# Kernel tuning notes

Hardware: AMD Instinct MI355X
Metric: run time of the kernel (lower is better)

## Reference

```python
import jax, jax.numpy as jnp
import numpy as np

B, S, D = 4, 2048, 1024
H = 16
DH = D // H  # 64
THETA = 10000.0


def setup_inputs() -> dict:
    key = jax.random.key(0)
    ks = jax.random.split(key, 7)
    scale = 1.0 / np.sqrt(D)
    return {
        "Q": jax.random.normal(ks[0], (B, S, D), dtype=jnp.float32),
        "K": jax.random.normal(ks[1], (B, S, D), dtype=jnp.float32),
        "V": jax.random.normal(ks[2], (B, S, D), dtype=jnp.float32),
        "Wq": jax.random.normal(ks[3], (D, D), dtype=jnp.float32) * scale,
        "Wk": jax.random.normal(ks[4], (D, D), dtype=jnp.float32) * scale,
        "Wv": jax.random.normal(ks[5], (D, D), dtype=jnp.float32) * scale,
        "Wo": jax.random.normal(ks[6], (D, D), dtype=jnp.float32) * scale,
    }


def _rope_tables(seq_len, d_head, theta, dtype):
    inv_freq = 1.0 / theta ** (jnp.arange(0, d_head, 2, dtype=jnp.float32) / d_head)
    ang = jnp.arange(seq_len, dtype=jnp.float32)[:, None] * inv_freq[None, :]  # [S, DH/2]
    return jnp.sin(ang).astype(dtype), jnp.cos(ang).astype(dtype)


def _apply_rope(x, sin, cos):
    # x: [B, H, S, DH]; sin/cos: [S, DH/2] broadcast over B,H
    x1 = x[..., 0::2]
    x2 = x[..., 1::2]
    x1r = x1 * cos - x2 * sin
    x2r = x1 * sin + x2 * cos
    return jnp.stack([x1r, x2r], axis=-1).reshape(x.shape)


def reference(Q, K, V, Wq, Wk, Wv, Wo):
    seq_len = Q.shape[-2]
    q = Q @ Wq.T
    k = K @ Wk.T
    v = V @ Wv.T

    def split(x):  # [B, S, D] -> [B, H, S, DH]
        return x.reshape(x.shape[0], seq_len, H, DH).transpose(0, 2, 1, 3)

    qh, kh, vh = split(q), split(k), split(v)

    sin, cos = _rope_tables(seq_len, DH, THETA, qh.dtype)
    qh = _apply_rope(qh, sin, cos)
    kh = _apply_rope(kh, sin, cos)

    # attention in fp32 (matches original cast)
    qf = qh.astype(jnp.float32)
    kf = kh.astype(jnp.float32)
    vf = vh.astype(jnp.float32)
    scale = 1.0 / np.sqrt(DH)
    scores = jnp.einsum('bhqd,bhkd->bhqk', qf, kf) * scale
    causal = jnp.tril(jnp.ones((seq_len, seq_len), dtype=bool))
    scores = jnp.where(causal, scores, -jnp.inf)
    attn = jax.nn.softmax(scores, axis=-1)
    out_h = jnp.einsum('bhqk,bhkd->bhqd', attn, vf).astype(Q.dtype)

    out = out_h.transpose(0, 2, 1, 3).reshape(Q.shape[0], seq_len, D)
    return out @ Wo.T
```

## Files before the change

kernel.cpp:

```cpp
#include <hip/hip_runtime.h>
#include <hip/hip_bf16.h>
#include <cmath>

#define B_ 4
#define S_ 2048
#define D_ 1024
#define H_ 16
#define DH_ 64

typedef __bf16 bf16_t;
typedef __bf16 bf16x8 __attribute__((ext_vector_type(8)));
typedef __bf16 bf16x4 __attribute__((ext_vector_type(4)));
typedef float f32x4 __attribute__((ext_vector_type(4)));

static __device__ __forceinline__ f32x4 mfma16(bf16x8 a, bf16x8 b, f32x4 c) {
    return __builtin_amdgcn_mfma_f32_16x16x32_bf16(a, b, c, 0, 0, 0);
}

static __device__ __forceinline__ float fast_exp2(float x) {
#if __has_builtin(__builtin_amdgcn_exp2f)
    return __builtin_amdgcn_exp2f(x);
#else
    float r; asm("v_exp_f32 %0, %1" : "=v"(r) : "v"(x)); return r;
#endif
}

static __device__ __forceinline__ void glds16(const void* g, void* l) {
    __builtin_amdgcn_global_load_lds(
        (const __attribute__((address_space(1))) unsigned int*)g,
        (__attribute__((address_space(3))) unsigned int*)l, 16, 0, 0);
}

__global__ __launch_bounds__(256)
void prep_kernel(const float* __restrict__ Wq, const float* __restrict__ Wk,
                 const float* __restrict__ Wv, const float* __restrict__ Wo,
                 bf16_t* __restrict__ Wb, float2* __restrict__ tab)
{
    int bid = blockIdx.x;
    if (bid < 256) {
        int idx = bid * 256 + threadIdx.x;
        int s = idx >> 5, i = idx & 31;
        float inv = powf(10000.f, -(2.f * i) / 64.f);
        float ang = (float)s * inv;
        tab[idx] = make_float2(sinf(ang), cosf(ang));
    } else {
        int i = (bid - 256) * 256 + threadIdx.x;
        int t = i >> 17, j = i & 131071;
        const float* src = (t == 0) ? Wq : (t == 1) ? Wk : (t == 2) ? Wv : Wo;
        const float4* s = (const float4*)(src + (size_t)j * 8);
        float4 a = s[0], b = s[1];
        bf16x8 v = { (__bf16)a.x, (__bf16)a.y, (__bf16)a.z, (__bf16)a.w,
                     (__bf16)b.x, (__bf16)b.y, (__bf16)b.z, (__bf16)b.w };
        *(bf16x8*)(Wb + (size_t)i * 8) = v;
    }
}

template<int EPI>
__global__ __launch_bounds__(256)
void proj_kernel(const float* __restrict__ X, const bf16_t* __restrict__ W,
                 bf16_t* __restrict__ dst, const float2* __restrict__ tab)
{
    __shared__ bf16x8 lA[2][128 * 8];
    __shared__ bf16x8 lB[2][128 * 8];
    const int tid = threadIdx.x;
    const int gm0 = blockIdx.x * 128;
    const int gn0 = blockIdx.y * 128;
    const int wid = tid >> 6, lane = tid & 63;
    const int lr = lane & 15, lh = lane >> 4;
    const int wm = (wid >> 1) * 64, wn = (wid & 1) * 64;

    int arow[4], aslot[4];
    const float* abase[4];
    #pragma unroll
    for (int i = 0; i < 4; ++i) {
        int slot = i * 256 + tid;
        int row = slot >> 3, s = slot & 7, c = s ^ (row & 7);
        arow[i] = row; aslot[i] = s;
        abase[i] = X + (size_t)(gm0 + row) * D_ + c * 8;
    }
    const bf16_t* bsrc[4]; int bbase[4];
    #pragma unroll
    for (int i = 0; i < 4; ++i) {
        int base = wid * 64 + i * 256;
        int slot = base + lane;
        int row = slot >> 3, s = slot & 7, c = s ^ (row & 7);
        bbase[i] = base;
        bsrc[i] = W + (size_t)(gn0 + row) * D_ + c * 8;
    }

    float4 av0[4], av1[4];
    #pragma unroll
    for (int i = 0; i < 4; ++i) {
        av0[i] = *(const float4*)(abase[i]);
        av1[i] = *(const float4*)(abase[i] + 4);
    }
    #pragma unroll
    for (int i = 0; i < 4; ++i) glds16(bsrc[i], &lB[0][bbase[i]]);
    #pragma unroll
    for (int i = 0; i < 4; ++i) {
        lA[0][arow[i] * 8 + aslot[i]] = bf16x8{
            (__bf16)av0[i].x, (__bf16)av0[i].y, (__bf16)av0[i].z, (__bf16)av0[i].w,
            (__bf16)av1[i].x, (__bf16)av1[i].y, (__bf16)av1[i].z, (__bf16)av1[i].w };
    }
    __syncthreads();

    f32x4 acc[4][4] = {};
    int cur = 0;

    #pragma unroll 1
    for (int kt = 0; kt < D_ / 64; ++kt) {
        const int nxt = cur ^ 1;
        if (kt + 1 < D_ / 64) {
            #pragma unroll
            for (int i = 0; i < 4; ++i)
                glds16(bsrc[i] + (kt + 1) * 64, &lB[nxt][bbase[i]]);
            #pragma unroll
            for (int i = 0; i < 4; ++i) {
                av0[i] = *(const float4*)(abase[i] + (kt + 1) * 64);
                av1[i] = *(const float4*)(abase[i] + (kt + 1) * 64 + 4);
            }
        }
        #pragma unroll
        for (int ks = 0; ks < 2; ++ks) {
            bf16x8 af[4], bfr[4];
            int kh8 = ks * 4 + lh;
            #pragma unroll
            for (int mi = 0; mi < 4; ++mi) { int r = wm + mi * 16 + lr; af[mi]  = lA[cur][r * 8 + (kh8 ^ (r & 7))]; }
            #pragma unroll
            for (int ni = 0; ni < 4; ++ni) { int r = wn + ni * 16 + lr; bfr[ni] = lB[cur][r * 8 + (kh8 ^ (r & 7))]; }
            #pragma unroll
            for (int mi = 0; mi < 4; ++mi)
                #pragma unroll
                for (int ni = 0; ni < 4; ++ni)
                    acc[mi][ni] = mfma16(af[mi], bfr[ni], acc[mi][ni]);
        }
        if (kt + 1 < D_ / 64) {
            #pragma unroll
            for (int i = 0; i < 4; ++i) {
                lA[nxt][arow[i] * 8 + aslot[i]] = bf16x8{
                    (__bf16)av0[i].x, (__bf16)av0[i].y, (__bf16)av0[i].z, (__bf16)av0[i].w,
                    (__bf16)av1[i].x, (__bf16)av1[i].y, (__bf16)av1[i].z, (__bf16)av1[i].w };
            }
        }
        __syncthreads();
        cur = nxt;
    }

    #pragma unroll
    for (int mi = 0; mi < 4; ++mi) {
        #pragma unroll
        for (int j = 0; j < 4; ++j) {
            int m = gm0 + wm + mi * 16 + lh * 4 + j;
            int b = m >> 11, s = m & (S_ - 1);
            #pragma unroll
            for (int ni = 0; ni < 4; ++ni) {
                int n = gn0 + wn + ni * 16 + lr;
                int h = n >> 6, dh = n & 63;
                float x = acc[mi][ni][j];
                if (EPI == 0) {
                    float p = __shfl_xor(x, 1);
                    float2 sc = tab[s * 32 + (dh >> 1)];
                    float r = (dh & 1) ? (p * sc.x + x * sc.y)
                                       : (x * sc.y - p * sc.x);
                    dst[(((size_t)b * H_ + h) * S_ + s) * DH_ + dh] = (bf16_t)r;
                } else {
                    dst[(((size_t)b * H_ + h) * DH_ + dh) * S_ + s] = (bf16_t)x;
                }
            }
        }
    }
}

__global__ __launch_bounds__(256, 6)
void attn_kernel(const bf16_t* __restrict__ qh, const bf16_t* __restrict__ kh,
                 const bf16_t* __restrict__ vT, bf16_t* __restrict__ O)
{
    __shared__ bf16x8 lK[64 * 8];
    __shared__ bf16x8 lV[64 * 8];
    __shared__ bf16x8 lP8[4][128];
    const int tid = threadIdx.x, wid = tid >> 6, lane = tid & 63;
    const int lr = lane & 15, lh = lane >> 4;
    const int bh = blockIdx.x & 63;
    const int t  = 31 - (blockIdx.x >> 6);
    const bf16_t* Qp = qh + (size_t)bh * S_ * DH_;
    const bf16_t* Kp = kh + (size_t)bh * S_ * DH_;
    const bf16_t* Vp = vT + (size_t)bh * DH_ * S_;
    char* lP = (char*)lP8[wid];
    const int b = bh >> 4, h = bh & 15;
    const float QSCALE = 0.125f * 1.44269504f;
    const int wq = t * 64 + wid * 16;

    bf16x8 qf[2];
    #pragma unroll
    for (int ks = 0; ks < 2; ++ks) {
        bf16x8 q8 = *(const bf16x8*)(Qp + (size_t)(wq + lr) * DH_ + ks * 32 + lh * 8);
        #pragma unroll
        for (int e = 0; e < 8; ++e) q8[e] = (__bf16)((float)q8[e] * QSCALE);
        qf[ks] = q8;
    }

    f32x4 accO[4] = {};
    float mrun = -1e30f, lrun = 0.f;
    const int nkt = t + 1;

    #pragma unroll 1
    for (int kt = 0; kt < nkt; ++kt) {
        __syncthreads();
        #pragma unroll
        for (int i = 0; i < 2; ++i) {
            int base = i * 256 + (wid << 6);
            int slot = base + lane;
            int row = slot >> 3, s = slot & 7, c = s ^ (row & 7);
            glds16(Kp + (size_t)(kt * 64 + row) * DH_ + c * 8, &lK[base]);
            glds16(Vp + (size_t)row * S_ + kt * 64 + c * 8, &lV[base]);
        }
        __syncthreads();

        f32x4 sc[4] = {};
        __builtin_amdgcn_s_setprio(1);
        #pragma unroll
        for (int ks = 0; ks < 2; ++ks) {
            int kh8 = ks * 4 + lh;
            #pragma unroll
            for (int kvi = 0; kvi < 4; ++kvi) {
                int r = kvi * 16 + lr;
                bf16x8 kf = lK[r * 8 + (kh8 ^ (r & 7))];
                sc[kvi] = mfma16(kf, qf[ks], sc[kvi]);
            }
        }
        __builtin_amdgcn_s_setprio(0);

        const int kvb = kt * 64 + 4 * lh;
        const int qg = wq + lr;
        float pv[16];
        if (kt == t) {
            #pragma unroll
            for (int kvi = 0; kvi < 4; ++kvi)
                #pragma unroll
                for (int j = 0; j < 4; ++j) {
                    float x = sc[kvi][j];
                    if ((kvb + kvi * 16 + j) > qg) x = -1e30f;
                    pv[kvi * 4 + j] = x;
                }
        } else {
            #pragma unroll
            for (int kvi = 0; kvi < 4; ++kvi)
                #pragma unroll
                for (int j = 0; j < 4; ++j) pv[kvi * 4 + j] = sc[kvi][j];
        }

        float t0 = fmaxf(fmaxf(pv[0],  pv[1]),  pv[2]);
        float t1 = fmaxf(fmaxf(pv[3],  pv[4]),  pv[5]);
        float t2 = fmaxf(fmaxf(pv[6],  pv[7]),  pv[8]);
        float t3 = fmaxf(fmaxf(pv[9],  pv[10]), pv[11]);
        float t4 = fmaxf(fmaxf(pv[12], pv[13]), pv[14]);
        float u0 = fmaxf(fmaxf(t0, t1), t2);
        float u1 = fmaxf(fmaxf(t3, t4), pv[15]);
        float mxp = fmaxf(u0, u1);

        float mnew = mrun;
        bool skip = __all(mxp <= mrun + 8.0f);
        if (!skip) {
            float mx = fmaxf(mxp, __shfl_xor(mxp, 16));
            mx = fmaxf(mx, __shfl_xor(mx, 32));
            mnew = fmaxf(mrun, mx);
            float rs = fast_exp2(mrun - mnew);
            mrun = mnew;
            lrun *= rs;
            #pragma unroll
            for (int j = 0; j < 4; ++j) {
                float rj = __shfl(rs, 4 * lh + j);
                #pragma unroll
                for (int ni = 0; ni < 4; ++ni) accO[ni][j] *= rj;
            }
        }
        #pragma unroll
        for (int i = 0; i < 16; ++i) pv[i] = fast_exp2(pv[i] - mnew);
        float s8[8], s4v[4];
        #pragma unroll
        for (int i = 0; i < 8; ++i) s8[i] = pv[i] + pv[i + 8];
        #pragma unroll
        for (int i = 0; i < 4; ++i) s4v[i] = s8[i] + s8[i + 4];
        lrun += (s4v[0] + s4v[1]) + (s4v[2] + s4v[3]);

        #pragma unroll
        for (int kvi = 0; kvi < 4; ++kvi) {
            bf16x4 hv = { (__bf16)pv[kvi * 4 + 0], (__bf16)pv[kvi * 4 + 1],
                          (__bf16)pv[kvi * 4 + 2], (__bf16)pv[kvi * 4 + 3] };
            int slot = 2 * kvi + (lh >> 1);
            *(bf16x4*)(lP + lr * 128 + ((slot ^ (lr & 7)) * 16) + (lh & 1) * 8) = hv;
        }

        __builtin_amdgcn_s_setprio(1);
        #pragma unroll
        for (int ks = 0; ks < 2; ++ks) {
            int kh8 = ks * 4 + lh;
            int slot = 4 * ks + lh;
            bf16x8 pf = *(const bf16x8*)(lP + lr * 128 + ((slot ^ (lr & 7)) * 16));
            #pragma unroll
            for (int ni = 0; ni < 4; ++ni) {
                int r = ni * 16 + lr;
                bf16x8 vf = lV[r * 8 + (kh8 ^ (r & 7))];
                accO[ni] = mfma16(pf, vf, accO[ni]);
            }
        }
        __builtin_amdgcn_s_setprio(0);
    }

    lrun += __shfl_xor(lrun, 16);
    lrun += __shfl_xor(lrun, 32);

    #pragma unroll
    for (int j = 0; j < 4; ++j) {
        int s = wq + 4 * lh + j;
        float inv = 1.f / __shfl(lrun, 4 * lh + j);
        #pragma unroll
        for (int ni = 0; ni < 4; ++ni) {
            int dh = ni * 16 + lr;
            O[((size_t)(b * S_ + s)) * D_ + h * DH_ + dh] = (bf16_t)(accO[ni][j] * inv);
        }
    }
}

__global__ __launch_bounds__(256)
void out_kernel(const bf16_t* __restrict__ A, const bf16_t* __restrict__ W,
                float* __restrict__ out)
{
    __shared__ bf16x8 lA[2][128 * 8];
    __shared__ bf16x8 lB[2][128 * 8];
    const int tid = threadIdx.x;
    const int gm0 = blockIdx.x * 128;
    const int gn0 = blockIdx.y * 128;
    const int wid = tid >> 6, lane = tid & 63;
    const int lr = lane & 15, lh = lane >> 4;
    const int wm = (wid >> 1) * 64, wn = (wid & 1) * 64;

    const bf16_t* asrc[4]; const bf16_t* bsrc[4]; int sbase[4];
    #pragma unroll
    for (int i = 0; i < 4; ++i) {
        int base = wid * 64 + i * 256;
        int slot = base + lane;
        int row = slot >> 3, s = slot & 7, c = s ^ (row & 7);
        sbase[i] = base;
        asrc[i] = A + (size_t)(gm0 + row) * D_ + c * 8;
        bsrc[i] = W + (size_t)(gn0 + row) * D_ + c * 8;
    }

    #pragma unroll
    for (int i = 0; i < 4; ++i) {
        glds16(asrc[i], &lA[0][sbase[i]]);
        glds16(bsrc[i], &lB[0][sbase[i]]);
    }
    __syncthreads();

    f32x4 acc[4][4] = {};
    int cur = 0;

    #pragma unroll 1
    for (int kt = 0; kt < D_ / 64; ++kt) {
        const int nxt = cur ^ 1;
        if (kt + 1 < D_ / 64) {
            #pragma unroll
            for (int i = 0; i < 4; ++i) {
                glds16(asrc[i] + (kt + 1) * 64, &lA[nxt][sbase[i]]);
                glds16(bsrc[i] + (kt + 1) * 64, &lB[nxt][sbase[i]]);
            }
        }
        #pragma unroll
        for (int ks = 0; ks < 2; ++ks) {
            bf16x8 af[4], bfr[4];
            int kh = ks * 4 + lh;
            #pragma unroll
            for (int mi = 0; mi < 4; ++mi) { int r = wm + mi * 16 + lr; af[mi]  = lA[cur][r * 8 + (kh ^ (r & 7))]; }
            #pragma unroll
            for (int ni = 0; ni < 4; ++ni) { int r = wn + ni * 16 + lr; bfr[ni] = lB[cur][r * 8 + (kh ^ (r & 7))]; }
            #pragma unroll
            for (int mi = 0; mi < 4; ++mi)
                #pragma unroll
                for (int ni = 0; ni < 4; ++ni)
                    acc[mi][ni] = mfma16(af[mi], bfr[ni], acc[mi][ni]);
        }
        __syncthreads();
        cur = nxt;
    }

    #pragma unroll
    for (int mi = 0; mi < 4; ++mi)
        #pragma unroll
        for (int j = 0; j < 4; ++j) {
            int m = gm0 + wm + mi * 16 + lh * 4 + j;
            #pragma unroll
            for (int ni = 0; ni < 4; ++ni) {
                int n = gn0 + wn + ni * 16 + lr;
                out[(size_t)m * D_ + n] = acc[mi][ni][j];
            }
        }
}

extern "C" void kernel_launch(void* const* d_in, const int* in_sizes, int n_in,
                              void* d_out, int out_size, void* d_ws, size_t ws_size,
                              hipStream_t stream)
{
    const float* Q  = (const float*)d_in[0];
    const float* K  = (const float*)d_in[1];
    const float* V  = (const float*)d_in[2];
    const float* Wq = (const float*)d_in[3];
    const float* Wk = (const float*)d_in[4];
    const float* Wv = (const float*)d_in[5];
    const float* Wo = (const float*)d_in[6];
    float* out = (float*)d_out;

    char* ws = (char*)d_ws;
    const size_t MB = 1024 * 1024;
    bf16_t* qh  = (bf16_t*)(ws);
    bf16_t* khb = (bf16_t*)(ws + 16 * MB);
    bf16_t* vT  = (bf16_t*)(ws + 32 * MB);
    bf16_t* Ob  = (bf16_t*)(ws + 48 * MB);
    bf16_t* Wb  = (bf16_t*)(ws + 64 * MB);
    float2* tab = (float2*)(ws + 72 * MB);

    prep_kernel<<<2304, 256, 0, stream>>>(Wq, Wk, Wv, Wo, Wb, tab);

    dim3 g(64, 8);
    proj_kernel<0><<<g, 256, 0, stream>>>(Q, Wb + 0 * 1048576, qh, tab);
    proj_kernel<0><<<g, 256, 0, stream>>>(K, Wb + 1 * 1048576, khb, tab);
    proj_kernel<1><<<g, 256, 0, stream>>>(V, Wb + 2 * 1048576, vT, tab);

    attn_kernel<<<2048, 256, 0, stream>>>(qh, khb, vT, Ob);

    out_kernel<<<dim3(64, 8), 256, 0, stream>>>(Ob, Wb + 3 * 1048576, out);
}
```

Baseline: 175.2 us.

## Prefetch next K/V tile into registers to overlap loads with compute

Replaces the direct global-to-LDS loads issued at the top of each KV iteration with a register prefetch. The next tile's K and V are loaded into VGPRs while the current tile is being computed, then stored to LDS at the start of the next iteration. The goal is to hide global memory latency behind the MFMA and softmax work. In exchange it uses more registers and goes through VGPRs instead of direct LDS loads. It also relies on a raw s_barrier at the end of the loop to protect LDS reuse, which may not wait for outstanding LDS operations the way __syncthreads does.

Result: slower. 208.4 us (+18.9%).

```diff
diff --git a/kernel.cpp b/kernel.cpp
--- a/kernel.cpp
+++ b/kernel.cpp
@@ -190,6 +190,17 @@
     const float QSCALE = 0.125f * 1.44269504f;
     const int wq = t * 64 + wid * 16;
 
+    int sslot[2];
+    const bf16_t* kga[2]; const bf16_t* vga[2];
+    #pragma unroll
+    for (int i = 0; i < 2; ++i) {
+        int slot = i * 256 + (wid << 6) + lane;
+        int row = slot >> 3, s = slot & 7, c = s ^ (row & 7);
+        sslot[i] = slot;
+        kga[i] = Kp + (size_t)row * DH_ + c * 8;
+        vga[i] = Vp + (size_t)row * S_ + c * 8;
+    }
+
     bf16x8 qf[2];
     #pragma unroll
     for (int ks = 0; ks < 2; ++ks) {
@@ -203,18 +214,29 @@
     float mrun = -1e30f, lrun = 0.f;
     const int nkt = t + 1;
 
+    bf16x8 kreg[2], vreg[2];
+    #pragma unroll
+    for (int i = 0; i < 2; ++i) {
+        kreg[i] = *(const bf16x8*)(kga[i]);
+        vreg[i] = *(const bf16x8*)(vga[i]);
+    }
+
     #pragma unroll 1
     for (int kt = 0; kt < nkt; ++kt) {
+        #pragma unroll
+        for (int i = 0; i < 2; ++i) {
+            lK[sslot[i]] = kreg[i];
+            lV[sslot[i]] = vreg[i];
+        }
         __syncthreads();
-        #pragma unroll
-        for (int i = 0; i < 2; ++i) {
-            int base = i * 256 + (wid << 6);
-            int slot = base + lane;
-            int row = slot >> 3, s = slot & 7, c = s ^ (row & 7);
-            glds16(Kp + (size_t)(kt * 64 + row) * DH_ + c * 8, &lK[base]);
-            glds16(Vp + (size_t)row * S_ + kt * 64 + c * 8, &lV[base]);
-        }
-        __syncthreads();
+
+        if (kt + 1 < nkt) {
+            #pragma unroll
+            for (int i = 0; i < 2; ++i) {
+                kreg[i] = *(const bf16x8*)(kga[i] + (size_t)(kt + 1) * 64 * DH_);
+                vreg[i] = *(const bf16x8*)(vga[i] + (size_t)(kt + 1) * 64);
+            }
+        }
 
         f32x4 sc[4] = {};
         __builtin_amdgcn_s_setprio(1);
@@ -305,6 +327,8 @@
             }
         }
         __builtin_amdgcn_s_setprio(0);
+
+        __builtin_amdgcn_s_barrier();
     }
 
     lrun += __shfl_xor(lrun, 16);
```
